# Kernel tuning notes

Measured on AMD Instinct MI355X. Metric: run time of the kernel, lower is better.

Reference implementation:

```python
import jax, jax.numpy as jnp
import numpy as np

N_NODES = 100000
N_EDGES = 1600000
IN_DIM = 128
HID_DIM = 64


def setup_inputs() -> dict:
    key = jax.random.key(0)
    ks = jax.random.split(key, 8)
    feat = jax.random.normal(ks[0], (N_NODES, IN_DIM), dtype=jnp.float32)
    # xavier-normal-like scaling for gcn weights
    w1 = jax.random.normal(ks[1], (IN_DIM, HID_DIM), dtype=jnp.float32) * np.sqrt(2.0 / (IN_DIM + HID_DIM))
    w2 = jax.random.normal(ks[2], (HID_DIM, HID_DIM), dtype=jnp.float32) * np.sqrt(2.0 / (HID_DIM + HID_DIM))
    conv_w = jax.random.normal(ks[3], (2, 1, 3), dtype=jnp.float32) * np.sqrt(2.0 / 3.0)
    conv_b = jax.random.uniform(ks[4], (2,), dtype=jnp.float32, minval=-1.0 / np.sqrt(3.0), maxval=1.0 / np.sqrt(3.0))
    ref_radius = jnp.zeros((1,), dtype=jnp.float32)
    src = jax.random.randint(ks[5], (N_EDGES,), 0, N_NODES, dtype=jnp.int32)
    dst = jax.random.randint(ks[6], (N_EDGES,), 0, N_NODES, dtype=jnp.int32)
    return {"feat": feat, "w1": w1, "w2": w2, "conv_w": conv_w, "conv_b": conv_b,
            "ref_radius": ref_radius, "src": src, "dst": dst}


def _dropout(h, key, p=0.5):
    keep = jax.random.bernoulli(key, 1.0 - p, h.shape)
    return jnp.where(keep, h / (1.0 - p), 0.0)


def _gcn(h, w, norm, src2, dst2, n, pre_matmul):
    # norm-scale -> (matmul) -> copy_src/sum scatter -> (matmul) -> norm-scale -> relu
    h = h * norm[:, None]
    if pre_matmul:  # in_feats > out_feats branch
        h = h @ w
        agg = jax.ops.segment_sum(h[src2], dst2, num_segments=n)
    else:
        agg = jax.ops.segment_sum(h[src2], dst2, num_segments=n)
        agg = agg @ w
    rst = agg * norm[:, None]
    return jax.nn.relu(rst)


def reference(feat, w1, w2, conv_w, conv_b, ref_radius, src, dst):
    n = feat.shape[0]
    # dgl.add_self_loop
    loops = jnp.arange(n, dtype=src.dtype)
    src2 = jnp.concatenate([src, loops])
    dst2 = jnp.concatenate([dst, loops])
    deg = jax.ops.segment_sum(jnp.ones_like(dst2, dtype=jnp.float32), dst2, num_segments=n)
    norm = jnp.clip(deg, 1.0, None) ** -0.5  # [n]

    dkey = jax.random.key(42)
    k1, k2 = jax.random.split(dkey)

    h = _gcn(feat, w1, norm, src2, dst2, n, pre_matmul=True)   # 128 > 64
    h = _dropout(h, k1)
    h = _gcn(h, w2, norm, src2, dst2, n, pre_matmul=False)     # 64 == 64
    h = _dropout(h, k2)

    # conv1d: [n, hid] -> [n, 1, hid] -> [n, 2, hid-2] -> [n, 2*(hid-2)]
    x = h[:, None, :]
    y = jax.lax.conv_general_dilated(x, conv_w, window_strides=(1,), padding='VALID',
                                     dimension_numbers=('NCH', 'OIH', 'NCH'))
    y = y + conv_b[None, :, None]
    h = y.reshape(n, -1)

    # hypersphere: distance of each node feature from the centroid vs ref radius
    o = jnp.mean(h, axis=0)
    radius = jnp.sqrt(jnp.sum((h - o + 1e-6) ** 2, axis=1))  # F.pairwise_distance eps=1e-6
    dis = jnp.clip(radius - ref_radius, 1e-4, 1.0 - 1e-4)
    return dis, ref_radius
```

## Files before the change

kernel.cpp:

```cpp
#include <hip/hip_runtime.h>
#include <stdint.h>

#define HID 64
#define INDIM 128
#define NBK 512
#define NBLK 512
#define EPBCAP 3200
#define BK3CAP 8192

typedef __attribute__((ext_vector_type(8))) short bf16x8;
typedef __attribute__((ext_vector_type(4))) float f32x4;
typedef __attribute__((ext_vector_type(2))) float f32x2;

__host__ __device__ __forceinline__ void tf2x32(uint32_t k0, uint32_t k1,
                                                uint32_t x0, uint32_t x1,
                                                uint32_t& o0, uint32_t& o1) {
  uint32_t ks2 = k0 ^ k1 ^ 0x1BD11BDAu;
#define ROTL(v, r) (((v) << (r)) | ((v) >> (32 - (r))))
#define RND(r) { x0 += x1; x1 = ROTL(x1, r); x1 ^= x0; }
  x0 += k0; x1 += k1;
  RND(13) RND(15) RND(26) RND(6)
  x0 += k1; x1 += ks2 + 1u;
  RND(17) RND(29) RND(16) RND(24)
  x0 += ks2; x1 += k0 + 2u;
  RND(13) RND(15) RND(26) RND(6)
  x0 += k0; x1 += k1 + 3u;
  RND(17) RND(29) RND(16) RND(24)
  x0 += k1; x1 += ks2 + 4u;
  RND(13) RND(15) RND(26) RND(6)
  x0 += ks2; x1 += k0 + 5u;
  o0 = x0; o1 = x1;
#undef RND
#undef ROTL
}

__device__ __forceinline__ float tf_uniform(uint32_t ka, uint32_t kb, uint32_t j) {
  uint32_t o0, o1;
  tf2x32(ka, kb, 0u, j, o0, o1);
  uint32_t bits = o0 ^ o1;
  uint32_t f = (bits >> 9) | 0x3f800000u;
  return __uint_as_float(f) - 1.0f;
}

__device__ __forceinline__ unsigned short f2bf(float f) {
  uint32_t x = __float_as_uint(f);
  uint32_t r = (x + 0x7fffu + ((x >> 16) & 1u)) >> 16;
  return (unsigned short)r;
}

__device__ __forceinline__ float bf2f_lo(uint32_t u) { return __uint_as_float(u << 16); }
__device__ __forceinline__ float bf2f_hi(uint32_t u) { return __uint_as_float(u & 0xffff0000u); }

__device__ __forceinline__ unsigned char f2fp8(float v) {
  return (unsigned char)(__builtin_amdgcn_cvt_pk_fp8_f32(v, 0.f, 0, false) & 0xff);
}

__global__ __launch_bounds__(256) void binsort_k(const int* __restrict__ src,
                                                 const int* __restrict__ dst,
                                                 uint32_t* __restrict__ sorted,
                                                 int* __restrict__ blockoff2,
                                                 int E, int EPB, int NB) {
  __shared__ uint32_t lbuf[EPBCAP];
  __shared__ int dbuf[EPBCAP];
  __shared__ int ha[NBK], hb[NBK], cursor[NBK];
  int b = blockIdx.x, t = threadIdx.x;
  int e0 = b * EPB;
  int e1 = e0 + EPB; if (e1 > E) e1 = E;
  int m = e1 - e0;
  ha[t] = 0; ha[t + 256] = 0;
  __syncthreads();
  for (int i = t; i < m; i += 256) {
    int d = dst[e0 + i];
    dbuf[i] = d;
    atomicAdd(&ha[d >> 8], 1);
  }
  __syncthreads();
  int* cur = ha; int* nxt = hb;
  for (int off = 1; off < 512; off <<= 1) {
    int i0 = t, i1 = t + 256;
    int v0 = cur[i0] + ((i0 >= off) ? cur[i0 - off] : 0);
    int v1 = cur[i1] + ((i1 >= off) ? cur[i1 - off] : 0);
    __syncthreads();
    nxt[i0] = v0; nxt[i1] = v1;
    __syncthreads();
    int* tmp = cur; cur = nxt; nxt = tmp;
  }
  for (int i = t; i < NB; i += 256) {
    int ex = (i == 0) ? 0 : cur[i - 1];
    cursor[i] = ex;
    blockoff2[(size_t)i * NBLK + b] = ex;
  }
  if (t == 0) blockoff2[(size_t)NB * NBLK + b] = m;
  __syncthreads();
  for (int i = t; i < m; i += 256) {
    int d = dbuf[i], s = src[e0 + i];
    int pos = atomicAdd(&cursor[d >> 8], 1);
    lbuf[pos] = ((uint32_t)s << 8) | (uint32_t)(d & 255);
  }
  __syncthreads();
  for (int i = t; i < m; i += 256) sorted[e0 + i] = lbuf[i];
}

__global__ __launch_bounds__(NBLK) void boff_k(const int* __restrict__ blockoff2,
                                               int* __restrict__ destoff,
                                               int* __restrict__ totals, int NB) {
  __shared__ int sa[NBK], sb[NBK];
  int k = blockIdx.x, t = threadIdx.x;
  int len = blockoff2[(size_t)(k + 1) * NBLK + t] - blockoff2[(size_t)k * NBLK + t];
  sa[t] = len;
  __syncthreads();
  int* cur = sa; int* nxt = sb;
  for (int off = 1; off < NBLK; off <<= 1) {
    int v = cur[t] + ((t >= off) ? cur[t - off] : 0);
    __syncthreads();
    nxt[t] = v;
    __syncthreads();
    int* tmp = cur; cur = nxt; nxt = tmp;
  }
  destoff[(size_t)k * NBLK + t] = cur[t] - len;
  if (t == NBLK - 1) totals[k] = cur[t];
}

__global__ __launch_bounds__(512) void bscan_k(const int* __restrict__ totals,
                                               int* __restrict__ bucketstart,
                                               float* __restrict__ colsum,
                                               int NB, int E) {
  __shared__ int sa[NBK], sb[NBK];
  int t = threadIdx.x;
  int v = (t < NB) ? totals[t] : 0;
  sa[t] = v;
  __syncthreads();
  int* cur = sa; int* nxt = sb;
  for (int off = 1; off < 512; off <<= 1) {
    int x = cur[t] + ((t >= off) ? cur[t - off] : 0);
    __syncthreads();
    nxt[t] = x;
    __syncthreads();
    int* tmp = cur; cur = nxt; nxt = tmp;
  }
  if (t < NB) bucketstart[t] = cur[t] - v;
  if (t == 0) bucketstart[NB] = E;
  if (t < HID) colsum[t] = 0.f;
}

__global__ __launch_bounds__(256) void csrbuild_k(const uint32_t* __restrict__ sorted,
                                                  const int* __restrict__ blockoff2,
                                                  const int* __restrict__ destoff,
                                                  const int* __restrict__ bucketstart,
                                                  int* __restrict__ rowstart,
                                                  int* __restrict__ csr,
                                                  float* __restrict__ norm,
                                                  int NB, int n, int E, int EPB) {
  __shared__ uint32_t ebuf[BK3CAP];
  __shared__ int sa[256], sb[256], cursor[256];
  int bid = blockIdx.x, t = threadIdx.x;
  int xcd = bid & 7, sub = bid >> 3;
  int q = NB >> 3, r = NB & 7;
  int k = (xcd < r ? xcd * (q + 1) : r * (q + 1) + (xcd - r) * q) + sub;
  int s0 = bucketstart[k], s1 = bucketstart[k + 1];
  int M = s1 - s0;
  for (int b = t; b < NBLK; b += 256) {
    int sb_ = blockoff2[(size_t)k * NBLK + b];
    int se_ = blockoff2[(size_t)(k + 1) * NBLK + b];
    int dd = destoff[(size_t)k * NBLK + b];
    const uint32_t* sp = sorted + (size_t)b * EPB;
    for (int i = sb_; i < se_; i++) ebuf[dd + (i - sb_)] = sp[i];
  }
  cursor[t] = 0;
  __syncthreads();
  for (int i = t; i < M; i += 256) atomicAdd(&cursor[ebuf[i] & 255], 1);
  __syncthreads();
  int cnt = cursor[t];
  sa[t] = cnt;
  int* cur = sa; int* nxt = sb;
  __syncthreads();
  for (int off = 1; off < 256; off <<= 1) {
    int v = cur[t] + ((t >= off) ? cur[t - off] : 0);
    __syncthreads();
    nxt[t] = v;
    __syncthreads();
    int* tmp = cur; cur = nxt; nxt = tmp;
  }
  int localrow = cur[t] - cnt;
  int node = k * 256 + t;
  if (node < n) {
    rowstart[node] = s0 + localrow;
    norm[node] = rsqrtf((float)(cnt + 1));
  }
  if (k == NB - 1 && t == 255) rowstart[n] = E;
  cursor[t] = localrow;
  __syncthreads();
  for (int i = t; i < M; i += 256) {
    uint32_t pe = ebuf[i];
    int pos = atomicAdd(&cursor[pe & 255], 1);
    csr[s0 + pos] = (int)(pe >> 8);
  }
}

__global__ __launch_bounds__(256) void wcvt_k(const float* __restrict__ w1,
                                              const float* __restrict__ w2,
                                              unsigned short* __restrict__ w1t,
                                              unsigned short* __restrict__ w2t) {
  int i = blockIdx.x * 256 + threadIdx.x;
  if (i < INDIM * HID) {
    int c = i >> 7, k = i & 127;
    w1t[i] = f2bf(w1[k * HID + c]);
  } else {
    int j = i - INDIM * HID;
    if (j < HID * HID) {
      int c = j >> 6, k = j & 63;
      w2t[j] = f2bf(w2[k * HID + c]);
    }
  }
}

__global__ __launch_bounds__(256) void gemm1(const float* __restrict__ feat,
                                             const unsigned short* __restrict__ w1t,
                                             const float* __restrict__ norm,
                                             unsigned char* __restrict__ h0, int n) {
  int t = threadIdx.x;
  int wv = t >> 6, lane = t & 63;
  int strip = blockIdx.x * 4 + wv;
  if (strip * 16 >= n) return;
  int m = lane & 15, q = lane >> 4;
  bf16x8 Bf[4][4];
#pragma unroll
  for (int kc = 0; kc < 4; kc++)
#pragma unroll
    for (int ct = 0; ct < 4; ct++)
      Bf[kc][ct] = *(const bf16x8*)(w1t + (ct * 16 + m) * INDIM + kc * 32 + q * 8);
  const float* arow = feat + (size_t)(strip * 16 + m) * INDIM;
  bf16x8 Af[4];
#pragma unroll
  for (int kc = 0; kc < 4; kc++) {
    const float* pa = arow + kc * 32 + q * 8;
    bf16x8 a;
#pragma unroll
    for (int j = 0; j < 8; j++) a[j] = (short)f2bf(pa[j]);
    Af[kc] = a;
  }
  f32x4 acc[4] = {{0.f,0.f,0.f,0.f},{0.f,0.f,0.f,0.f},{0.f,0.f,0.f,0.f},{0.f,0.f,0.f,0.f}};
#pragma unroll
  for (int kc = 0; kc < 4; kc++)
#pragma unroll
    for (int ct = 0; ct < 4; ct++)
      acc[ct] = __builtin_amdgcn_mfma_f32_16x16x32_bf16(Af[kc], Bf[kc][ct], acc[ct], 0, 0, 0);
#pragma unroll
  for (int r = 0; r < 4; r++) {
    int row = strip * 16 + q * 4 + r;
    float nm = norm[row];
#pragma unroll
    for (int ct = 0; ct < 4; ct++)
      h0[(size_t)row * HID + ct * 16 + m] = f2fp8(acc[ct][r] * nm);
  }
}

template <int MODE>
__global__ __launch_bounds__(256) void gather_k(const uint32_t* __restrict__ h8,
                                                void* __restrict__ outp,
                                                const int* __restrict__ rowstart,
                                                const int* __restrict__ csr,
                                                const float* __restrict__ norm,
                                                int n, uint32_t ka, uint32_t kb) {
  int wid = (int)((blockIdx.x * 256u + threadIdx.x) >> 6);
  int d0 = wid * 4;
  if (d0 >= n) return;
  int lane = threadIdx.x & 63;
  int g = lane >> 4, c4 = lane & 15;
  int g4 = g << 2;

  int rr = d0 + (lane < 4 ? lane : 4);
  if (rr > n) rr = n;
  int rsl = rowstart[rr];
  int r0[5];
#pragma unroll
  for (int i = 0; i < 5; ++i) r0[i] = __shfl(rsl, i);
  int L[4];
#pragma unroll
  for (int i = 0; i < 4; ++i) L[i] = r0[i + 1] - r0[i];

  int selfrow = d0 + g; if (selfrow >= n) selfrow = d0;
  uint32_t uself = h8[(size_t)selfrow * 16 + c4];

  int idx[4];
#pragma unroll
  for (int i = 0; i < 4; ++i) {
    int la = L[i] < 32 ? L[i] : 32;
    idx[i] = (lane < la) ? csr[r0[i] + lane] : 0;
  }

  uint32_t u[4][8];
#pragma unroll
  for (int i = 0; i < 4; ++i) {
#pragma unroll
    for (int t = 0; t < 8; ++t) {
      int s = __builtin_amdgcn_ds_bpermute(16 * t + g4, idx[i]);
      u[i][t] = (4 * t + g < L[i]) ? h8[(size_t)(uint32_t)s * 16 + c4] : 0u;
    }
  }

  f32x2 al[4], ah[4];
#pragma unroll
  for (int i = 0; i < 4; ++i) { al[i] = (f32x2){0.f, 0.f}; ah[i] = (f32x2){0.f, 0.f}; }
#pragma unroll
  for (int i = 0; i < 4; ++i) {
#pragma unroll
    for (int t = 0; t < 8; ++t) {
      al[i] += __builtin_amdgcn_cvt_pk_f32_fp8((int)u[i][t], false);
      ah[i] += __builtin_amdgcn_cvt_pk_f32_fp8((int)u[i][t], true);
    }
  }

#pragma unroll
  for (int i = 0; i < 4; ++i) {
    if (L[i] > 32) {
      for (int e0 = 32; e0 < L[i]; e0 += 4) {
        int e = e0 + g;
        uint32_t uu = 0u;
        if (e < L[i]) {
          int s = csr[r0[i] + e];
          uu = h8[(size_t)(uint32_t)s * 16 + c4];
        }
        al[i] += __builtin_amdgcn_cvt_pk_f32_fp8((int)uu, false);
        ah[i] += __builtin_amdgcn_cvt_pk_f32_fp8((int)uu, true);
      }
    }
  }

  f32x2 sl, sh, rl2, rh2;
  sl = (g & 1) ? al[0] : al[1];
  sh = (g & 1) ? ah[0] : ah[1];
  rl2.x = __shfl_xor(sl.x, 16); rl2.y = __shfl_xor(sl.y, 16);
  rh2.x = __shfl_xor(sh.x, 16); rh2.y = __shfl_xor(sh.y, 16);
  f32x2 fABl = ((g & 1) ? al[1] : al[0]) + rl2;
  f32x2 fABh = ((g & 1) ? ah[1] : ah[0]) + rh2;
  sl = (g & 1) ? al[2] : al[3];
  sh = (g & 1) ? ah[2] : ah[3];
  rl2.x = __shfl_xor(sl.x, 16); rl2.y = __shfl_xor(sl.y, 16);
  rh2.x = __shfl_xor(sh.x, 16); rh2.y = __shfl_xor(sh.y, 16);
  f32x2 fCDl = ((g & 1) ? al[3] : al[2]) + rl2;
  f32x2 fCDh = ((g & 1) ? ah[3] : ah[2]) + rh2;
  sl = (g & 2) ? fABl : fCDl;
  sh = (g & 2) ? fABh : fCDh;
  rl2.x = __shfl_xor(sl.x, 32); rl2.y = __shfl_xor(sl.y, 32);
  rh2.x = __shfl_xor(sh.x, 32); rh2.y = __shfl_xor(sh.y, 32);
  f32x2 tl = ((g & 2) ? fCDl : fABl) + rl2;
  f32x2 th = ((g & 2) ? fCDh : fABh) + rh2;

  tl += __builtin_amdgcn_cvt_pk_f32_fp8((int)uself, false);
  th += __builtin_amdgcn_cvt_pk_f32_fp8((int)uself, true);

  int d = d0 + g;
  float a0 = tl.x, a1 = tl.y, a2 = th.x, a3 = th.y;
  if (MODE == 0) {
    uint32_t jb = (uint32_t)d0 * 64u + (uint32_t)lane;
    float u0 = tf_uniform(ka, kb, jb);
    float u1 = tf_uniform(ka, kb, jb + 64u);
    float u2 = tf_uniform(ka, kb, jb + 128u);
    float u3 = tf_uniform(ka, kb, jb + 192u);
    unsigned long long kp0 = __ballot(u0 < 0.5f);
    unsigned long long kp1 = __ballot(u1 < 0.5f);
    unsigned long long kp2 = __ballot(u2 < 0.5f);
    unsigned long long kp3 = __ballot(u3 < 0.5f);
    unsigned long long keep = (g & 2) ? ((g & 1) ? kp3 : kp2)
                                      : ((g & 1) ? kp1 : kp0);
    uint32_t kb4 = (uint32_t)(keep >> (4 * c4)) & 15u;
    float nm = norm[d < n ? d : d0];
    float v0 = fmaxf(a0 * nm, 0.f), v1 = fmaxf(a1 * nm, 0.f);
    float v2 = fmaxf(a2 * nm, 0.f), v3 = fmaxf(a3 * nm, 0.f);
    float s2 = 2.f * nm;
    v0 = (kb4 & 1u) ? v0 * s2 : 0.f;
    v1 = (kb4 & 2u) ? v1 * s2 : 0.f;
    v2 = (kb4 & 4u) ? v2 * s2 : 0.f;
    v3 = (kb4 & 8u) ? v3 * s2 : 0.f;
    if (d < n) {
      int o = __builtin_amdgcn_cvt_pk_fp8_f32(v0, v1, 0, false);
      o = __builtin_amdgcn_cvt_pk_fp8_f32(v2, v3, o, true);
      ((uint32_t*)outp)[(size_t)d * 16 + c4] = (uint32_t)o;
    }
  } else {
    if (d < n) {
      uint2 w;
      w.x = (uint32_t)f2bf(a0) | ((uint32_t)f2bf(a1) << 16);
      w.y = (uint32_t)f2bf(a2) | ((uint32_t)f2bf(a3) << 16);
      ((uint2*)outp)[(size_t)d * 16 + c4] = w;
    }
  }
}

__global__ __launch_bounds__(256) void gemm2(const unsigned short* __restrict__ aggbf,
                                             const unsigned short* __restrict__ w2t,
                                             const float* __restrict__ norm,
                                             unsigned short* __restrict__ h2, int n,
                                             uint32_t ka, uint32_t kb) {
  int t = threadIdx.x;
  int wv = t >> 6, lane = t & 63;
  int strip = blockIdx.x * 4 + wv;
  if (strip * 16 >= n) return;
  int m = lane & 15, q = lane >> 4;
  bf16x8 Bf[2][4];
#pragma unroll
  for (int kc = 0; kc < 2; kc++)
#pragma unroll
    for (int ct = 0; ct < 4; ct++)
      Bf[kc][ct] = *(const bf16x8*)(w2t + (ct * 16 + m) * HID + kc * 32 + q * 8);
  const unsigned short* arow = aggbf + (size_t)(strip * 16 + m) * HID;
  bf16x8 Af[2];
#pragma unroll
  for (int kc = 0; kc < 2; kc++)
    Af[kc] = *(const bf16x8*)(arow + kc * 32 + q * 8);
  f32x4 acc[4] = {{0.f,0.f,0.f,0.f},{0.f,0.f,0.f,0.f},{0.f,0.f,0.f,0.f},{0.f,0.f,0.f,0.f}};
#pragma unroll
  for (int kc = 0; kc < 2; kc++)
#pragma unroll
    for (int ct = 0; ct < 4; ct++)
      acc[ct] = __builtin_amdgcn_mfma_f32_16x16x32_bf16(Af[kc], Bf[kc][ct], acc[ct], 0, 0, 0);
#pragma unroll
  for (int r = 0; r < 4; r++) {
    int row = strip * 16 + q * 4 + r;
    float nm = norm[row];
#pragma unroll
    for (int ct = 0; ct < 4; ct++) {
      int col = ct * 16 + m;
      float v = fmaxf(acc[ct][r] * nm, 0.f);
      float u = tf_uniform(ka, kb, (uint32_t)row * 64u + (uint32_t)col);
      v = (u < 0.5f) ? v * 2.f : 0.f;
      h2[(size_t)row * HID + col] = f2bf(v);
    }
  }
}

__global__ __launch_bounds__(256) void colsum_k(const uint32_t* __restrict__ h2u,
                                                float* __restrict__ colsum, int n) {
  int t = threadIdx.x;
  int cp = t & 31;
  int rg = t >> 5;
  float sx = 0.f, sy = 0.f;
  for (int r = blockIdx.x * 8 + rg; r < n; r += gridDim.x * 8) {
    uint32_t u = h2u[(size_t)r * 32 + cp];
    sx += bf2f_lo(u); sy += bf2f_hi(u);
  }
  __shared__ float red[8][HID];
  red[rg][2 * cp] = sx; red[rg][2 * cp + 1] = sy;
  __syncthreads();
  if (t < HID) {
    float v = 0.f;
#pragma unroll
    for (int i = 0; i < 8; i++) v += red[i][t];
    atomicAdd(&colsum[t], v);
  }
}

__global__ __launch_bounds__(128) void final_k(const uint32_t* __restrict__ h2u,
                                               const float* __restrict__ colsum,
                                               const float* __restrict__ conv_w,
                                               const float* __restrict__ conv_b,
                                               const float* __restrict__ ref_radius,
                                               float* __restrict__ out, int n) {
  __shared__ float rows[128 * 67];
  __shared__ float omean[124];
  __shared__ float cm[HID];
  int t = threadIdx.x;
  int node0 = blockIdx.x * 128;
  if (t < HID) cm[t] = colsum[t] * (1.0f / (float)n);
  for (int idx = t; idx < 128 * 32; idx += 128) {
    int r = idx >> 5, cpi = idx & 31;
    int node = node0 + r;
    uint32_t u = (node < n) ? h2u[(size_t)node * 32 + cpi] : 0u;
    rows[r * 67 + 2 * cpi] = bf2f_lo(u);
    rows[r * 67 + 2 * cpi + 1] = bf2f_hi(u);
  }
  __syncthreads();
  if (t < 124) {
    int o = t / 62, i = t % 62;
    omean[t] = conv_b[o] + conv_w[o * 3] * cm[i] + conv_w[o * 3 + 1] * cm[i + 1] +
               conv_w[o * 3 + 2] * cm[i + 2];
  }
  __syncthreads();
  int node = node0 + t;
  if (node < n) {
    float r0[HID];
#pragma unroll
    for (int k = 0; k < HID; k++) r0[k] = rows[t * 67 + k];
    float w00 = conv_w[0], w01 = conv_w[1], w02 = conv_w[2];
    float w10 = conv_w[3], w11 = conv_w[4], w12 = conv_w[5];
    float b0 = conv_b[0], b1 = conv_b[1];
    float acc = 0.f;
#pragma unroll
    for (int i = 0; i < 62; i++) {
      float y0 = b0 + w00 * r0[i] + w01 * r0[i + 1] + w02 * r0[i + 2];
      float d0 = y0 - omean[i] + 1e-6f;
      acc += d0 * d0;
      float y1 = b1 + w10 * r0[i] + w11 * r0[i + 1] + w12 * r0[i + 2];
      float d1 = y1 - omean[62 + i] + 1e-6f;
      acc += d1 * d1;
    }
    float radius = sqrtf(acc);
    float dis = fminf(fmaxf(radius - ref_radius[0], 1e-4f), 1.f - 1e-4f);
    out[node] = dis;
  }
  if (blockIdx.x == 0 && t == 0) out[n] = ref_radius[0];
}

extern "C" void kernel_launch(void* const* d_in, const int* in_sizes, int n_in,
                              void* d_out, int out_size, void* d_ws, size_t ws_size,
                              hipStream_t stream) {
  const float* feat = (const float*)d_in[0];
  const float* w1 = (const float*)d_in[1];
  const float* w2 = (const float*)d_in[2];
  const float* conv_w = (const float*)d_in[3];
  const float* conv_b = (const float*)d_in[4];
  const float* ref_radius = (const float*)d_in[5];
  const int* src = (const int*)d_in[6];
  const int* dst = (const int*)d_in[7];
  int n = in_sizes[0] / INDIM;
  int E = in_sizes[6];
  float* out = (float*)d_out;

  int NB = (n + 255) >> 8;
  int EPB = (E + NBLK - 1) / NBLK;

  char* p = (char*)d_ws;
  auto carve = [&](size_t bytes) { void* r = (void*)p; p += (bytes + 255) & ~(size_t)255; return r; };
  float* norm = (float*)carve((size_t)n * 4);
  float* colsum = (float*)carve(HID * 4);
  int* rowstart = (int*)carve(((size_t)n + 1) * 4);
  int* bucketstart = (int*)carve(((size_t)NB + 1) * 4);
  int* totals = (int*)carve((size_t)NB * 4);
  int* blockoff2 = (int*)carve((size_t)(NB + 1) * NBLK * 4);
  int* destoff = (int*)carve((size_t)NB * NBLK * 4);
  uint32_t* sorted = (uint32_t*)carve((size_t)E * 4);
  int* csr = (int*)carve((size_t)E * 4);
  unsigned short* w1t = (unsigned short*)carve((size_t)INDIM * HID * 2);
  unsigned short* w2t = (unsigned short*)carve((size_t)HID * HID * 2);
  unsigned char* H0f8 = (unsigned char*)carve((size_t)n * HID);
  unsigned char* Tf8 = (unsigned char*)carve((size_t)n * HID);
  unsigned short* Abf = (unsigned short*)carve((size_t)n * HID * 2);
  unsigned short* H2bf = (unsigned short*)carve((size_t)n * HID * 2);

  uint32_t k1a, k1b, k2a, k2b;
  tf2x32(0u, 42u, 0u, 0u, k1a, k1b);
  tf2x32(0u, 42u, 0u, 1u, k2a, k2b);

  int gatherB = (n + 15) / 16;
  int stripB = ((n + 15) / 16 + 3) / 4;

  binsort_k<<<NBLK, 256, 0, stream>>>(src, dst, sorted, blockoff2, E, EPB, NB);
  boff_k<<<NB, NBLK, 0, stream>>>(blockoff2, destoff, totals, NB);
  bscan_k<<<1, 512, 0, stream>>>(totals, bucketstart, colsum, NB, E);
  csrbuild_k<<<NB, 256, 0, stream>>>(sorted, blockoff2, destoff, bucketstart, rowstart, csr, norm, NB, n, E, EPB);
  wcvt_k<<<(INDIM * HID + HID * HID + 255) / 256, 256, 0, stream>>>(w1, w2, w1t, w2t);
  gemm1<<<stripB, 256, 0, stream>>>(feat, w1t, norm, H0f8, n);
  gather_k<0><<<gatherB, 256, 0, stream>>>((const uint32_t*)H0f8, Tf8, rowstart, csr, norm, n, k1a, k1b);
  gather_k<1><<<gatherB, 256, 0, stream>>>((const uint32_t*)Tf8, Abf, rowstart, csr, norm, n, 0u, 0u);
  gemm2<<<stripB, 256, 0, stream>>>(Abf, w2t, norm, H2bf, n, k2a, k2b);
  colsum_k<<<256, 256, 0, stream>>>((const uint32_t*)H2bf, colsum, n);
  final_k<<<(n + 127) / 128, 128, 0, stream>>>((const uint32_t*)H2bf, colsum, conv_w, conv_b, ref_radius, out, n);
}
```

Baseline: 256.8 us.

## Fuse bucket offset scans into csrbuild and column sums into gemm2

The separate boff_k and bscan_k scan kernels are removed. Each csrbuild block now derives its own bucket start by reducing the per-block offsets below it and scans the 512 per-block lengths itself. The colsum kernel is folded into gemm2's epilogue using shuffle and shared-memory reductions plus atomics, and colsum zeroing moves into wcvt_k, which now runs first. This drops three launches and one re-read of H2. In exchange every csrbuild block does redundant scan work, and there are more atomics on colsum (one per gemm2 block) and fp32 accumulation-order differences.

Result: no change. 258.8 us (+0.8%).

```diff
diff --git a/kernel.cpp b/kernel.cpp
--- a/kernel.cpp
+++ b/kernel.cpp
@@ -101,70 +101,52 @@
   for (int i = t; i < m; i += 256) sorted[e0 + i] = lbuf[i];
 }
 
-__global__ __launch_bounds__(NBLK) void boff_k(const int* __restrict__ blockoff2,
-                                               int* __restrict__ destoff,
-                                               int* __restrict__ totals, int NB) {
-  __shared__ int sa[NBK], sb[NBK];
-  int k = blockIdx.x, t = threadIdx.x;
-  int len = blockoff2[(size_t)(k + 1) * NBLK + t] - blockoff2[(size_t)k * NBLK + t];
-  sa[t] = len;
-  __syncthreads();
-  int* cur = sa; int* nxt = sb;
-  for (int off = 1; off < NBLK; off <<= 1) {
-    int v = cur[t] + ((t >= off) ? cur[t - off] : 0);
-    __syncthreads();
-    nxt[t] = v;
-    __syncthreads();
-    int* tmp = cur; cur = nxt; nxt = tmp;
-  }
-  destoff[(size_t)k * NBLK + t] = cur[t] - len;
-  if (t == NBLK - 1) totals[k] = cur[t];
-}
-
-__global__ __launch_bounds__(512) void bscan_k(const int* __restrict__ totals,
-                                               int* __restrict__ bucketstart,
-                                               float* __restrict__ colsum,
-                                               int NB, int E) {
-  __shared__ int sa[NBK], sb[NBK];
-  int t = threadIdx.x;
-  int v = (t < NB) ? totals[t] : 0;
-  sa[t] = v;
-  __syncthreads();
-  int* cur = sa; int* nxt = sb;
-  for (int off = 1; off < 512; off <<= 1) {
-    int x = cur[t] + ((t >= off) ? cur[t - off] : 0);
-    __syncthreads();
-    nxt[t] = x;
-    __syncthreads();
-    int* tmp = cur; cur = nxt; nxt = tmp;
-  }
-  if (t < NB) bucketstart[t] = cur[t] - v;
-  if (t == 0) bucketstart[NB] = E;
-  if (t < HID) colsum[t] = 0.f;
-}
-
 __global__ __launch_bounds__(256) void csrbuild_k(const uint32_t* __restrict__ sorted,
                                                   const int* __restrict__ blockoff2,
-                                                  const int* __restrict__ destoff,
-                                                  const int* __restrict__ bucketstart,
                                                   int* __restrict__ rowstart,
                                                   int* __restrict__ csr,
                                                   float* __restrict__ norm,
                                                   int NB, int n, int E, int EPB) {
   __shared__ uint32_t ebuf[BK3CAP];
   __shared__ int sa[256], sb[256], cursor[256];
+  __shared__ int sc_[NBLK], sd_[NBLK];
   int bid = blockIdx.x, t = threadIdx.x;
   int xcd = bid & 7, sub = bid >> 3;
-  int q = NB >> 3, r = NB & 7;
-  int k = (xcd < r ? xcd * (q + 1) : r * (q + 1) + (xcd - r) * q) + sub;
-  int s0 = bucketstart[k], s1 = bucketstart[k + 1];
-  int M = s1 - s0;
-  for (int b = t; b < NBLK; b += 256) {
-    int sb_ = blockoff2[(size_t)k * NBLK + b];
-    int se_ = blockoff2[(size_t)(k + 1) * NBLK + b];
-    int dd = destoff[(size_t)k * NBLK + b];
-    const uint32_t* sp = sorted + (size_t)b * EPB;
-    for (int i = sb_; i < se_; i++) ebuf[dd + (i - sb_)] = sp[i];
+  int qq = NB >> 3, rr = NB & 7;
+  int k = (xcd < rr ? xcd * (qq + 1) : rr * (qq + 1) + (xcd - rr) * qq) + sub;
+
+  int b0 = t, b1 = t + 256;
+  int lo0 = blockoff2[(size_t)k * NBLK + b0];
+  int lo1 = blockoff2[(size_t)k * NBLK + b1];
+  int hi0 = blockoff2[(size_t)(k + 1) * NBLK + b0];
+  int hi1 = blockoff2[(size_t)(k + 1) * NBLK + b1];
+  int len0 = hi0 - lo0, len1 = hi1 - lo1;
+  sa[t] = lo0 + lo1;
+  sc_[b0] = len0; sc_[b1] = len1;
+  __syncthreads();
+  for (int off = 128; off > 0; off >>= 1) {
+    if (t < off) sa[t] += sa[t + off];
+    __syncthreads();
+  }
+  int s0 = sa[0];
+  int* cur = sc_; int* nxt = sd_;
+  for (int off = 1; off < NBLK; off <<= 1) {
+    int v0 = cur[b0] + ((b0 >= off) ? cur[b0 - off] : 0);
+    int v1 = cur[b1] + ((b1 >= off) ? cur[b1 - off] : 0);
+    __syncthreads();
+    nxt[b0] = v0; nxt[b1] = v1;
+    __syncthreads();
+    int* tmp = cur; cur = nxt; nxt = tmp;
+  }
+  int M = cur[NBLK - 1];
+  int dd0 = cur[b0] - len0, dd1 = cur[b1] - len1;
+  {
+    const uint32_t* sp = sorted + (size_t)b0 * EPB;
+    for (int i = lo0; i < hi0; i++) ebuf[dd0 + (i - lo0)] = sp[i];
+  }
+  {
+    const uint32_t* sp = sorted + (size_t)b1 * EPB;
+    for (int i = lo1; i < hi1; i++) ebuf[dd1 + (i - lo1)] = sp[i];
   }
   cursor[t] = 0;
   __syncthreads();
@@ -172,16 +154,16 @@
   __syncthreads();
   int cnt = cursor[t];
   sa[t] = cnt;
-  int* cur = sa; int* nxt = sb;
+  int* cu2 = sa; int* nx2 = sb;
   __syncthreads();
   for (int off = 1; off < 256; off <<= 1) {
-    int v = cur[t] + ((t >= off) ? cur[t - off] : 0);
-    __syncthreads();
-    nxt[t] = v;
-    __syncthreads();
-    int* tmp = cur; cur = nxt; nxt = tmp;
-  }
-  int localrow = cur[t] - cnt;
+    int v = cu2[t] + ((t >= off) ? cu2[t - off] : 0);
+    __syncthreads();
+    nx2[t] = v;
+    __syncthreads();
+    int* tmp = cu2; cu2 = nx2; nx2 = tmp;
+  }
+  int localrow = cu2[t] - cnt;
   int node = k * 256 + t;
   if (node < n) {
     rowstart[node] = s0 + localrow;
@@ -200,7 +182,9 @@
 __global__ __launch_bounds__(256) void wcvt_k(const float* __restrict__ w1,
                                               const float* __restrict__ w2,
                                               unsigned short* __restrict__ w1t,
-                                              unsigned short* __restrict__ w2t) {
+                                              unsigned short* __restrict__ w2t,
+                                              float* __restrict__ colsum) {
+  if (blockIdx.x == 0 && threadIdx.x < HID) colsum[threadIdx.x] = 0.f;
   int i = blockIdx.x * 256 + threadIdx.x;
   if (i < INDIM * HID) {
     int c = i >> 7, k = i & 127;
@@ -391,62 +375,63 @@
 __global__ __launch_bounds__(256) void gemm2(const unsigned short* __restrict__ aggbf,
                                              const unsigned short* __restrict__ w2t,
                                              const float* __restrict__ norm,
-                                             unsigned short* __restrict__ h2, int n,
+                                             unsigned short* __restrict__ h2,
+                                             float* __restrict__ colsum, int n,
                                              uint32_t ka, uint32_t kb) {
+  __shared__ float red[4][HID];
   int t = threadIdx.x;
   int wv = t >> 6, lane = t & 63;
   int strip = blockIdx.x * 4 + wv;
-  if (strip * 16 >= n) return;
   int m = lane & 15, q = lane >> 4;
-  bf16x8 Bf[2][4];
-#pragma unroll
-  for (int kc = 0; kc < 2; kc++)
-#pragma unroll
-    for (int ct = 0; ct < 4; ct++)
-      Bf[kc][ct] = *(const bf16x8*)(w2t + (ct * 16 + m) * HID + kc * 32 + q * 8);
-  const unsigned short* arow = aggbf + (size_t)(strip * 16 + m) * HID;
-  bf16x8 Af[2];
-#pragma unroll
-  for (int kc = 0; kc < 2; kc++)
-    Af[kc] = *(const bf16x8*)(arow + kc * 32 + q * 8);
-  f32x4 acc[4] = {{0.f,0.f,0.f,0.f},{0.f,0.f,0.f,0.f},{0.f,0.f,0.f,0.f},{0.f,0.f,0.f,0.f}};
-#pragma unroll
-  for (int kc = 0; kc < 2; kc++)
-#pragma unroll
-    for (int ct = 0; ct < 4; ct++)
-      acc[ct] = __builtin_amdgcn_mfma_f32_16x16x32_bf16(Af[kc], Bf[kc][ct], acc[ct], 0, 0, 0);
-#pragma unroll
-  for (int r = 0; r < 4; r++) {
-    int row = strip * 16 + q * 4 + r;
-    float nm = norm[row];
-#pragma unroll
-    for (int ct = 0; ct < 4; ct++) {
-      int col = ct * 16 + m;
-      float v = fmaxf(acc[ct][r] * nm, 0.f);
-      float u = tf_uniform(ka, kb, (uint32_t)row * 64u + (uint32_t)col);
-      v = (u < 0.5f) ? v * 2.f : 0.f;
-      h2[(size_t)row * HID + col] = f2bf(v);
-    }
-  }
-}
-
-__global__ __launch_bounds__(256) void colsum_k(const uint32_t* __restrict__ h2u,
-                                                float* __restrict__ colsum, int n) {
-  int t = threadIdx.x;
-  int cp = t & 31;
-  int rg = t >> 5;
-  float sx = 0.f, sy = 0.f;
-  for (int r = blockIdx.x * 8 + rg; r < n; r += gridDim.x * 8) {
-    uint32_t u = h2u[(size_t)r * 32 + cp];
-    sx += bf2f_lo(u); sy += bf2f_hi(u);
-  }
-  __shared__ float red[8][HID];
-  red[rg][2 * cp] = sx; red[rg][2 * cp + 1] = sy;
+  float cs[4] = {0.f, 0.f, 0.f, 0.f};
+  bool active = (strip * 16 < n);
+  if (active) {
+    bf16x8 Bf[2][4];
+#pragma unroll
+    for (int kc = 0; kc < 2; kc++)
+#pragma unroll
+      for (int ct = 0; ct < 4; ct++)
+        Bf[kc][ct] = *(const bf16x8*)(w2t + (ct * 16 + m) * HID + kc * 32 + q * 8);
+    const unsigned short* arow = aggbf + (size_t)(strip * 16 + m) * HID;
+    bf16x8 Af[2];
+#pragma unroll
+    for (int kc = 0; kc < 2; kc++)
+      Af[kc] = *(const bf16x8*)(arow + kc * 32 + q * 8);
+    f32x4 acc[4] = {{0.f,0.f,0.f,0.f},{0.f,0.f,0.f,0.f},{0.f,0.f,0.f,0.f},{0.f,0.f,0.f,0.f}};
+#pragma unroll
+    for (int kc = 0; kc < 2; kc++)
+#pragma unroll
+      for (int ct = 0; ct < 4; ct++)
+        acc[ct] = __builtin_amdgcn_mfma_f32_16x16x32_bf16(Af[kc], Bf[kc][ct], acc[ct], 0, 0, 0);
+#pragma unroll
+    for (int r = 0; r < 4; r++) {
+      int row = strip * 16 + q * 4 + r;
+      float nm = norm[row];
+#pragma unroll
+      for (int ct = 0; ct < 4; ct++) {
+        int col = ct * 16 + m;
+        float v = fmaxf(acc[ct][r] * nm, 0.f);
+        float u = tf_uniform(ka, kb, (uint32_t)row * 64u + (uint32_t)col);
+        v = (u < 0.5f) ? v * 2.f : 0.f;
+        h2[(size_t)row * HID + col] = f2bf(v);
+        cs[ct] += v;
+      }
+    }
+  }
+#pragma unroll
+  for (int ct = 0; ct < 4; ct++) {
+    cs[ct] += __shfl_xor(cs[ct], 16);
+    cs[ct] += __shfl_xor(cs[ct], 32);
+  }
+  if (q == 0) {
+    red[wv][m] = cs[0];
+    red[wv][16 + m] = cs[1];
+    red[wv][32 + m] = cs[2];
+    red[wv][48 + m] = cs[3];
+  }
   __syncthreads();
   if (t < HID) {
-    float v = 0.f;
-#pragma unroll
-    for (int i = 0; i < 8; i++) v += red[i][t];
+    float v = red[0][t] + red[1][t] + red[2][t] + red[3][t];
     atomicAdd(&colsum[t], v);
   }
 }
@@ -525,10 +510,7 @@
   float* norm = (float*)carve((size_t)n * 4);
   float* colsum = (float*)carve(HID * 4);
   int* rowstart = (int*)carve(((size_t)n + 1) * 4);
-  int* bucketstart = (int*)carve(((size_t)NB + 1) * 4);
-  int* totals = (int*)carve((size_t)NB * 4);
   int* blockoff2 = (int*)carve((size_t)(NB + 1) * NBLK * 4);
-  int* destoff = (int*)carve((size_t)NB * NBLK * 4);
   uint32_t* sorted = (uint32_t*)carve((size_t)E * 4);
   int* csr = (int*)carve((size_t)E * 4);
   unsigned short* w1t = (unsigned short*)carve((size_t)INDIM * HID * 2);
@@ -545,15 +527,12 @@
   int gatherB = (n + 15) / 16;
   int stripB = ((n + 15) / 16 + 3) / 4;
 
+  wcvt_k<<<(INDIM * HID + HID * HID + 255) / 256, 256, 0, stream>>>(w1, w2, w1t, w2t, colsum);
   binsort_k<<<NBLK, 256, 0, stream>>>(src, dst, sorted, blockoff2, E, EPB, NB);
-  boff_k<<<NB, NBLK, 0, stream>>>(blockoff2, destoff, totals, NB);
-  bscan_k<<<1, 512, 0, stream>>>(totals, bucketstart, colsum, NB, E);
-  csrbuild_k<<<NB, 256, 0, stream>>>(sorted, blockoff2, destoff, bucketstart, rowstart, csr, norm, NB, n, E, EPB);
-  wcvt_k<<<(INDIM * HID + HID * HID + 255) / 256, 256, 0, stream>>>(w1, w2, w1t, w2t);
+  csrbuild_k<<<NB, 256, 0, stream>>>(sorted, blockoff2, rowstart, csr, norm, NB, n, E, EPB);
   gemm1<<<stripB, 256, 0, stream>>>(feat, w1t, norm, H0f8, n);
   gather_k<0><<<gatherB, 256, 0, stream>>>((const uint32_t*)H0f8, Tf8, rowstart, csr, norm, n, k1a, k1b);
   gather_k<1><<<gatherB, 256, 0, stream>>>((const uint32_t*)Tf8, Abf, rowstart, csr, norm, n, 0u, 0u);
-  gemm2<<<stripB, 256, 0, stream>>>(Abf, w2t, norm, H2bf, n, k2a, k2b);
-  colsum_k<<<256, 256, 0, stream>>>((const uint32_t*)H2bf, colsum, n);
+  gemm2<<<stripB, 256, 0, stream>>>(Abf, w2t, norm, H2bf, colsum, n, k2a, k2b);
   final_k<<<(n + 127) / 128, 128, 0, stream>>>((const uint32_t*)H2bf, colsum, conv_w, conv_b, ref_radius, out, n);
 }
```
